# Performance work log

Measured on AMD Instinct MI355X. Metric: run time of the kernel, lower is better.

## Reference

```python
import jax, jax.numpy as jnp
import numpy as np

EPS = 1e-06
FOCUSING_FACTOR = 3


def setup_inputs() -> dict:
    key = jax.random.key(0)
    k1, k2, k3, k4, k5 = jax.random.split(key, 5)
    N, L, H, D = 8, 4096, 8, 64
    return {
        "queries": jax.random.normal(k1, (N, L, H, D), dtype=jnp.float32),
        "keys": jax.random.normal(k2, (N, L, H, D), dtype=jnp.float32),
        "values": jax.random.normal(k3, (N, L, H, D), dtype=jnp.float32),
        "scale_param": jnp.zeros((1, 1, 1, D), dtype=jnp.float32),
        "dwc_w": jax.random.normal(k4, (D, 1, 5, 5), dtype=jnp.float32) * 0.1,
        "dwc_b": jax.random.normal(k5, (D,), dtype=jnp.float32) * 0.1,
        "height": 64,
    }


def reference(queries, keys, values, scale_param, dwc_w, dwc_b, height):
    N, L, H, D = values.shape
    width = L // height

    scale = jax.nn.softplus(scale_param)  # [1,1,1,D]
    q = (jax.nn.relu(queries) + 1e-06) / scale
    k = (jax.nn.relu(keys) + 1e-06) / scale

    q_norm = jnp.linalg.norm(q, axis=-1, keepdims=True)
    k_norm = jnp.linalg.norm(k, axis=-1, keepdims=True)
    q = q ** FOCUSING_FACTOR
    k = k ** FOCUSING_FACTOR
    q = q / jnp.linalg.norm(q, axis=-1, keepdims=True) * q_norm
    k = k / jnp.linalg.norm(k, axis=-1, keepdims=True) * k_norm

    # linear attention: kv summary [N,H,D,D], normalizer z [N,L,H]
    kv = jnp.einsum("nshd,nshv->nhdv", k, values)
    z = 1.0 / (jnp.einsum("nlhd,nhd->nlh", q, k.sum(axis=1)) + EPS)
    o = jnp.einsum("nlhd,nhdv,nlh->nlhv", q, kv, z)

    # depthwise 5x5 conv on values: 'n (h w) heads d -> (n heads) d h w'
    vf = values.reshape(N, height, width, H, D)
    vf = vf.transpose(0, 3, 4, 1, 2).reshape(N * H, D, height, width)
    vf = jax.lax.conv_general_dilated(
        vf, dwc_w,
        window_strides=(1, 1), padding=((2, 2), (2, 2)),
        dimension_numbers=("NCHW", "OIHW", "NCHW"),
        feature_group_count=D,
    ) + dwc_b[None, :, None, None]
    vf = vf.reshape(N, H, D, height, width).transpose(0, 3, 4, 1, 2)
    vf = vf.reshape(N, L, H, D)

    return o + vf
```

## Files before the change

kernel.cpp:

```cpp
#include <hip/hip_runtime.h>

typedef __attribute__((ext_vector_type(8))) short short8;
typedef __attribute__((ext_vector_type(4))) float f32x4;

#define LSEQ   4096
#define NHEAD  8
#define DCH    64
#define HEIGHT 64
#define WIDTH  64

static __device__ __forceinline__ float bfu2f(unsigned short u) {
  return __uint_as_float(((unsigned int)u) << 16);
}
static __device__ __forceinline__ unsigned short f2bfu(float f) {
  unsigned int b = __float_as_uint(f);
  b += 0x7FFFu + ((b >> 16) & 1u);
  return (unsigned short)(b >> 16);
}
static __device__ __forceinline__ float ldf(const void* p, int i, int isbf) {
  return isbf ? bfu2f(((const unsigned short*)p)[i]) : ((const float*)p)[i];
}
static __device__ __forceinline__ float softplus_inv(float sp) {
  float s = (sp > 20.f) ? sp : log1pf(expf(sp));
  return 1.f / s;
}
static __device__ __forceinline__ void unpack2(unsigned int u, float& lo, float& hi) {
  lo = __uint_as_float(u << 16);
  hi = __uint_as_float(u & 0xFFFF0000u);
}
static __device__ __forceinline__ void load8(const void* p, int gi, int isbf, float o[8]) {
  if (isbf) {
    uint4 u = *(const uint4*)((const unsigned short*)p + gi);
    unpack2(u.x, o[0], o[1]); unpack2(u.y, o[2], o[3]);
    unpack2(u.z, o[4], o[5]); unpack2(u.w, o[6], o[7]);
  } else {
    const float4* f4 = (const float4*)((const float*)p + gi);
    float4 a = f4[0], b = f4[1];
    o[0]=a.x; o[1]=a.y; o[2]=a.z; o[3]=a.w;
    o[4]=b.x; o[5]=b.y; o[6]=b.z; o[7]=b.w;
  }
}
static __device__ __forceinline__ void row_reduce2(float& a, float& b) {
  #pragma unroll
  for (int m = 1; m < 8; m <<= 1) { a += __shfl_xor(a, m, 64); b += __shfl_xor(b, m, 64); }
}
static __device__ __forceinline__ float row_reduce1(float a) {
  #pragma unroll
  for (int m = 1; m < 8; m <<= 1) a += __shfl_xor(a, m, 64);
  return a;
}

__global__ void detect_kernel(const unsigned int* __restrict__ q, int* __restrict__ flag) {
  int lane = threadIdx.x & 63;
  int hits = 0;
  #pragma unroll
  for (int i = 0; i < 4; ++i) {
    unsigned int lo = q[lane * 4 + i] & 0xFFFFu;
    unsigned int e  = (lo >> 7) & 0xFFu;
    if (lo == 0u || (e >= 110u && e <= 140u)) hits++;
  }
  #pragma unroll
  for (int m = 1; m < 64; m <<= 1) hits += __shfl_xor(hits, m, 64);
  if (lane == 0) *flag = (hits > 128) ? 1 : 0;
}

__global__ __launch_bounds__(256) void kv_kernel(
    const void* __restrict__ keys, const void* __restrict__ values,
    const void* __restrict__ scale_param,
    float* __restrict__ kv_p, float* __restrict__ ksum_g,
    const int* __restrict__ flagp, int chunks, int rows)
{
  __shared__ __align__(16) unsigned short kfT[2][64 * 40];
  __shared__ __align__(16) unsigned short vvT[2][64 * 40];
  __shared__ float red[256];

  const int isbf = *flagp;
  const int b = blockIdx.x;
  const int chunk = b % chunks;
  const int nh = b / chunks;
  const int h = nh & 7, n = nh >> 3;
  const int t = threadIdx.x, lane = t & 63, wid = t >> 6;
  const int quad = lane >> 4, m16 = lane & 15;
  const int r = lane >> 3, c = lane & 7, d0 = c * 8;
  const int s_local = wid * 8 + r;
  const int sp = s_local ^ ((c & 3) << 3);

  float inv_s[8];
  #pragma unroll
  for (int i = 0; i < 8; ++i) inv_s[i] = softplus_inv(ldf(scale_param, d0 + i, isbf));

  f32x4 acc[4];
  #pragma unroll
  for (int mt = 0; mt < 4; ++mt) acc[mt] = (f32x4){0.f, 0.f, 0.f, 0.f};
  float ksum_acc[8];
  #pragma unroll
  for (int i = 0; i < 8; ++i) ksum_acc[i] = 0.f;

  const int nsub = rows >> 5;

  auto norm_k = [&](const float kraw[8], int buf) {
    float xv[8], yv[8], s2 = 0.f, s6 = 0.f;
    #pragma unroll
    for (int i = 0; i < 8; ++i) {
      xv[i] = (fmaxf(kraw[i], 0.f) + 1e-6f) * inv_s[i];
      s2 += xv[i] * xv[i];
    }
    #pragma unroll
    for (int i = 0; i < 8; ++i) {
      yv[i] = xv[i] * xv[i] * xv[i];
      s6 += yv[i] * yv[i];
    }
    row_reduce2(s2, s6);
    const float coef = sqrtf(s2 / s6);
    #pragma unroll
    for (int i = 0; i < 8; ++i) {
      float f = yv[i] * coef;
      ksum_acc[i] += f;
      kfT[buf][(d0 + i) * 40 + sp] = f2bfu(f);
    }
  };
  auto procb = [&](uint4 K, uint4 V, int buf) {
    float kraw[8];
    unpack2(K.x, kraw[0], kraw[1]); unpack2(K.y, kraw[2], kraw[3]);
    unpack2(K.z, kraw[4], kraw[5]); unpack2(K.w, kraw[6], kraw[7]);
    norm_k(kraw, buf);
    unsigned short vs8[8];
    *(uint4*)vs8 = V;
    #pragma unroll
    for (int i = 0; i < 8; ++i) vvT[buf][(d0 + i) * 40 + sp] = vs8[i];
  };
  auto mfma_step = [&](int buf) {
    const int v = wid * 16 + m16;
    short8 bfr = *(const short8*)&vvT[buf][v * 40 + (quad ^ ((v >> 3) & 3)) * 8];
    #pragma unroll
    for (int mt = 0; mt < 4; ++mt) {
      int d = mt * 16 + m16;
      short8 afr = *(const short8*)&kfT[buf][d * 40 + (quad ^ ((d >> 3) & 3)) * 8];
      acc[mt] = __builtin_amdgcn_mfma_f32_16x16x32_bf16(afr, bfr, acc[mt], 0, 0, 0);
    }
  };

  if (isbf) {
    const unsigned short* kp = (const unsigned short*)keys;
    const unsigned short* vp = (const unsigned short*)values;
    uint4 k0, k1, k2, k3, v0, v1, v2, v3;
    for (int g = 0; g < nsub; g += 4) {
      const int s = chunk * rows + g * 32 + s_local;
      const size_t gi = ((size_t)(n * LSEQ + s) * NHEAD + h) * DCH + d0;
      k0 = *(const uint4*)(kp + gi);
      v0 = *(const uint4*)(vp + gi);
      k1 = *(const uint4*)(kp + gi + 16384);
      v1 = *(const uint4*)(vp + gi + 16384);
      k2 = *(const uint4*)(kp + gi + 32768);
      v2 = *(const uint4*)(vp + gi + 32768);
      k3 = *(const uint4*)(kp + gi + 49152);
      v3 = *(const uint4*)(vp + gi + 49152);
      procb(k0, v0, 0); __syncthreads();
      mfma_step(0); procb(k1, v1, 1); __syncthreads();
      mfma_step(1); procb(k2, v2, 0); __syncthreads();
      mfma_step(0); procb(k3, v3, 1); __syncthreads();
      mfma_step(1);
    }
  } else {
    for (int sub = 0; sub < nsub; ++sub) {
      const int s = chunk * rows + sub * 32 + s_local;
      const int gi = ((n * LSEQ + s) * NHEAD + h) * DCH + d0;
      float kraw[8];
      load8(keys, gi, 0, kraw);
      norm_k(kraw, 0);
      float vraw[8];
      load8(values, gi, 0, vraw);
      #pragma unroll
      for (int i = 0; i < 8; ++i) vvT[0][(d0 + i) * 40 + sp] = f2bfu(vraw[i]);
      __syncthreads();
      mfma_step(0);
      __syncthreads();
    }
  }

  float* dst = kv_p + ((size_t)chunk * 64 + nh) * 4096;
  #pragma unroll
  for (int mt = 0; mt < 4; ++mt)
    #pragma unroll
    for (int rr = 0; rr < 4; ++rr) {
      int d = mt * 16 + quad * 4 + rr;
      dst[d * 64 + wid * 16 + m16] = acc[mt][rr];
    }

  #pragma unroll
  for (int i = 0; i < 8; ++i) {
    #pragma unroll
    for (int m = 8; m < 64; m <<= 1) ksum_acc[i] += __shfl_xor(ksum_acc[i], m, 64);
  }
  if (r == 0) {
    #pragma unroll
    for (int i = 0; i < 8; ++i) red[wid * 64 + d0 + i] = ksum_acc[i];
  }
  __syncthreads();
  if (t < 64) {
    float tot = red[t] + red[64 + t] + red[128 + t] + red[192 + t];
    atomicAdd(&ksum_g[nh * 64 + t], tot);
  }
}

__global__ __launch_bounds__(256) void reduce_kernel(
    const float* __restrict__ kv_p, unsigned short* __restrict__ kvb, int chunks)
{
  int cidx = blockIdx.x * 256 + threadIdx.x;
  int nh = cidx >> 12;
  int dv = cidx & 4095;
  int d = dv >> 6, v = dv & 63;
  float s = 0.f;
  for (int ch = 0; ch < chunks; ++ch)
    s += kv_p[((size_t)ch * 64 + nh) * 4096 + dv];
  kvb[(nh * 64 + v) * 64 + d] = f2bfu(s);
}

__global__ __launch_bounds__(256) void attn_kernel(
    const void* __restrict__ queries, const unsigned short* __restrict__ kvb,
    const float* __restrict__ ksum_g, const void* __restrict__ scale_param,
    void* __restrict__ out, const int* __restrict__ flagp)
{
  __shared__ __align__(16) unsigned short qf[64 * 72];

  const int isbf = *flagp;
  const int b = blockIdx.x;
  const int y = b & 63;
  const int nh = b >> 6;
  const int h = nh & 7, n = nh >> 3;
  const int t = threadIdx.x, lane = t & 63, wid = t >> 6;
  const int quad = lane >> 4, m16 = lane & 15;
  const int r = lane >> 3, c = lane & 7, d0 = c * 8;

  float inv_s[8];
  #pragma unroll
  for (int i = 0; i < 8; ++i) inv_s[i] = softplus_inv(ldf(scale_param, d0 + i, isbf));
  float ks[8];
  {
    float4 k0 = *(const float4*)&ksum_g[nh * 64 + d0];
    float4 k1 = *(const float4*)&ksum_g[nh * 64 + d0 + 4];
    ks[0]=k0.x; ks[1]=k0.y; ks[2]=k0.z; ks[3]=k0.w;
    ks[4]=k1.x; ks[5]=k1.y; ks[6]=k1.z; ks[7]=k1.w;
  }

  const unsigned short* kvrow = kvb + (nh * 64 + wid * 16 + m16) * 64;
  short8 bfr0 = *(const short8*)&kvrow[quad * 8];
  short8 bfr1 = *(const short8*)&kvrow[32 + quad * 8];

  #pragma unroll
  for (int batch = 0; batch < 2; ++batch) {
    int x = wid * 16 + batch * 8 + r;
    int gi = ((n * LSEQ + y * 64 + x) * NHEAD + h) * DCH + d0;
    float qraw[8];
    load8(queries, gi, isbf, qraw);
    float xv[8], yv[8], s2 = 0.f, s6 = 0.f;
    #pragma unroll
    for (int i = 0; i < 8; ++i) {
      xv[i] = (fmaxf(qraw[i], 0.f) + 1e-6f) * inv_s[i];
      s2 += xv[i] * xv[i];
    }
    #pragma unroll
    for (int i = 0; i < 8; ++i) {
      yv[i] = xv[i] * xv[i] * xv[i];
      s6 += yv[i] * yv[i];
    }
    row_reduce2(s2, s6);
    const float coef = sqrtf(s2 / s6);
    float f[8], dot = 0.f;
    #pragma unroll
    for (int i = 0; i < 8; ++i) { f[i] = yv[i] * coef; dot += f[i] * ks[i]; }
    dot = row_reduce1(dot);
    const float z = 1.f / (dot + 1e-6f);
    uint4 pk;
    pk.x = (unsigned int)f2bfu(f[0] * z) | ((unsigned int)f2bfu(f[1] * z) << 16);
    pk.y = (unsigned int)f2bfu(f[2] * z) | ((unsigned int)f2bfu(f[3] * z) << 16);
    pk.z = (unsigned int)f2bfu(f[4] * z) | ((unsigned int)f2bfu(f[5] * z) << 16);
    pk.w = (unsigned int)f2bfu(f[6] * z) | ((unsigned int)f2bfu(f[7] * z) << 16);
    *(uint4*)&qf[x * 72 + d0] = pk;
  }
  __syncthreads();

  const size_t obase = (((size_t)n * LSEQ + y * 64) * NHEAD + h) * DCH;
  #pragma unroll
  for (int mt = 0; mt < 4; ++mt) {
    f32x4 acc = (f32x4){0.f, 0.f, 0.f, 0.f};
    short8 a0 = *(const short8*)&qf[(mt * 16 + m16) * 72 + quad * 8];
    short8 a1 = *(const short8*)&qf[(mt * 16 + m16) * 72 + 32 + quad * 8];
    acc = __builtin_amdgcn_mfma_f32_16x16x32_bf16(a0, bfr0, acc, 0, 0, 0);
    acc = __builtin_amdgcn_mfma_f32_16x16x32_bf16(a1, bfr1, acc, 0, 0, 0);
    #pragma unroll
    for (int rr = 0; rr < 4; ++rr) {
      int x = mt * 16 + quad * 4 + rr;
      int v = wid * 16 + m16;
      size_t oi = obase + (size_t)x * (NHEAD * DCH) + v;
      if (isbf) ((unsigned short*)out)[oi] = f2bfu(acc[rr]);
      else      ((float*)out)[oi] = acc[rr];
    }
  }
}

__global__ __launch_bounds__(256) void conv_kernel(
    const void* __restrict__ values, const void* __restrict__ dwc_w,
    const void* __restrict__ dwc_b, void* __restrict__ out,
    const int* __restrict__ flagp)
{
  __shared__ __align__(16) unsigned short vs[8 * 64 * 32];
  __shared__ float wl[25 * 32];
  __shared__ float bl[32];

  const int isbf = *flagp;
  const int b = blockIdx.x;
  const int slab = b & 15;
  const int half = (b >> 4) & 1;
  const int nh = b >> 5;
  const int h = nh & 7, n = nh >> 3;
  const int y0 = slab * 4;
  const int t = threadIdx.x;

  for (int i = t; i < 800; i += 256) {
    int dloc = i / 25, tap = i - dloc * 25;
    wl[tap * 32 + dloc] = ldf(dwc_w, half * 800 + i, isbf);
  }
  if (t < 32) bl[t] = ldf(dwc_b, half * 32 + t, isbf);

  for (int it = t; it < 8 * 64 * 4; it += 256) {
    int j = it & 3;
    int xx = (it >> 2) & 63;
    int rr = it >> 8;
    int yy = y0 - 2 + rr;
    int swz = j ^ (xx & 3) ^ ((xx >> 2) & 3);
    unsigned short* dst = &vs[((rr * 64 + xx) * 32) + swz * 8];
    if (yy >= 0 && yy < HEIGHT) {
      int gi = ((n * LSEQ + yy * 64 + xx) * NHEAD + h) * DCH + half * 32 + j * 8;
      if (isbf) {
        *(uint4*)dst = *(const uint4*)((const unsigned short*)values + gi);
      } else {
        const float4* s4 = (const float4*)((const float*)values + gi);
        float4 f0 = s4[0], f1 = s4[1];
        dst[0] = f2bfu(f0.x); dst[1] = f2bfu(f0.y);
        dst[2] = f2bfu(f0.z); dst[3] = f2bfu(f0.w);
        dst[4] = f2bfu(f1.x); dst[5] = f2bfu(f1.y);
        dst[6] = f2bfu(f1.z); dst[7] = f2bfu(f1.w);
      }
    } else {
      uint4 z; z.x = z.y = z.z = z.w = 0u;
      *(uint4*)dst = z;
    }
  }
  __syncthreads();

  const int xx = t >> 2, jb = t & 3;
  float a[4][8];
  float bias8[8];
  {
    float4 b0 = *(const float4*)&bl[jb * 8];
    float4 b1 = *(const float4*)&bl[jb * 8 + 4];
    bias8[0]=b0.x; bias8[1]=b0.y; bias8[2]=b0.z; bias8[3]=b0.w;
    bias8[4]=b1.x; bias8[5]=b1.y; bias8[6]=b1.z; bias8[7]=b1.w;
  }
  #pragma unroll
  for (int rr = 0; rr < 4; ++rr)
    #pragma unroll
    for (int cc = 0; cc < 8; ++cc) a[rr][cc] = bias8[cc];

  for (int ky = 0; ky < 5; ++ky) {
    #pragma unroll
    for (int kx = 0; kx < 5; ++kx) {
      int xs = xx + kx - 2;
      if ((unsigned)xs < (unsigned)WIDTH) {
        float4 w0 = *(const float4*)&wl[(ky * 5 + kx) * 32 + jb * 8];
        float4 w1 = *(const float4*)&wl[(ky * 5 + kx) * 32 + jb * 8 + 4];
        int swz = jb ^ (xs & 3) ^ ((xs >> 2) & 3);
        #pragma unroll
        for (int rr = 0; rr < 4; ++rr) {
          uint4 pv = *(const uint4*)&vs[(((rr + ky) * 64 + xs) * 32) + swz * 8];
          float v0,v1,v2,v3,v4,v5,v6,v7;
          unpack2(pv.x, v0, v1); unpack2(pv.y, v2, v3);
          unpack2(pv.z, v4, v5); unpack2(pv.w, v6, v7);
          a[rr][0] += w0.x * v0; a[rr][1] += w0.y * v1;
          a[rr][2] += w0.z * v2; a[rr][3] += w0.w * v3;
          a[rr][4] += w1.x * v4; a[rr][5] += w1.y * v5;
          a[rr][6] += w1.z * v6; a[rr][7] += w1.w * v7;
        }
      }
    }
  }
  #pragma unroll
  for (int rr = 0; rr < 4; ++rr) {
    size_t oi = (((size_t)n * LSEQ + (y0 + rr) * 64 + xx) * NHEAD + h) * DCH
              + half * 32 + jb * 8;
    if (isbf) {
      unsigned short* op = (unsigned short*)out + oi;
      uint4 cur = *(uint4*)op;
      float c0,c1,c2,c3,c4,c5,c6,c7;
      unpack2(cur.x, c0, c1); unpack2(cur.y, c2, c3);
      unpack2(cur.z, c4, c5); unpack2(cur.w, c6, c7);
      uint4 res;
      res.x = (unsigned int)f2bfu(c0 + a[rr][0]) | ((unsigned int)f2bfu(c1 + a[rr][1]) << 16);
      res.y = (unsigned int)f2bfu(c2 + a[rr][2]) | ((unsigned int)f2bfu(c3 + a[rr][3]) << 16);
      res.z = (unsigned int)f2bfu(c4 + a[rr][4]) | ((unsigned int)f2bfu(c5 + a[rr][5]) << 16);
      res.w = (unsigned int)f2bfu(c6 + a[rr][6]) | ((unsigned int)f2bfu(c7 + a[rr][7]) << 16);
      *(uint4*)op = res;
    } else {
      float* op = (float*)out + oi;
      float4 o0 = *(float4*)op;
      float4 o1 = *(float4*)(op + 4);
      o0.x += a[rr][0]; o0.y += a[rr][1]; o0.z += a[rr][2]; o0.w += a[rr][3];
      o1.x += a[rr][4]; o1.y += a[rr][5]; o1.z += a[rr][6]; o1.w += a[rr][7];
      *(float4*)op = o0;
      *(float4*)(op + 4) = o1;
    }
  }
}

extern "C" void kernel_launch(void* const* d_in, const int* in_sizes, int n_in,
                              void* d_out, int out_size, void* d_ws, size_t ws_size,
                              hipStream_t stream) {
  int chunks = 32;
  while (chunks > 1) {
    size_t need = (size_t)chunks * 64 * 4096 * 4 + 64 * 4096 * 2 + 4096 * 4 + 64;
    if (need <= ws_size) break;
    chunks >>= 1;
  }
  const int rows = LSEQ / chunks;

  float* kv_p = (float*)d_ws;
  unsigned short* kvb = (unsigned short*)(kv_p + (size_t)chunks * 64 * 4096);
  float* ksum = (float*)(kvb + 64 * 4096);
  int* flag = (int*)(ksum + 4096);

  hipMemsetAsync(ksum, 0, 4096 * sizeof(float), stream);
  detect_kernel<<<1, 64, 0, stream>>>((const unsigned int*)d_in[0], flag);
  kv_kernel<<<64 * chunks, 256, 0, stream>>>(
      d_in[1], d_in[2], d_in[3], kv_p, ksum, flag, chunks, rows);
  reduce_kernel<<<1024, 256, 0, stream>>>(kv_p, kvb, chunks);
  attn_kernel<<<4096, 256, 0, stream>>>(
      d_in[0], kvb, ksum, d_in[3], d_out, flag);
  conv_kernel<<<64 * 32, 256, 0, stream>>>(
      d_in[2], d_in[4], d_in[5], d_out, flag);
}
```

Before: 315.6 us.

## Batch four sub-tiles per barrier in kv_kernel and halve chunk count

The kv_kernel now stages four 32-row sub-tiles into four LDS buffers and then runs one MFMA round over all of them. This replaces the per-sub-tile double-buffered ping-pong and cuts the barriers from four to two per group. The fp32 path is restructured the same way. Chunks drop from 32 to 16, which halves the partial kv buffers and reduce work but doubles the rows per block and halves the grid. LDS use doubles, and there is less overlap between normalization and MFMA.

```diff
diff --git a/kernel.cpp b/kernel.cpp
--- a/kernel.cpp
+++ b/kernel.cpp
@@ -70,8 +70,8 @@
     float* __restrict__ kv_p, float* __restrict__ ksum_g,
     const int* __restrict__ flagp, int chunks, int rows)
 {
-  __shared__ __align__(16) unsigned short kfT[2][64 * 40];
-  __shared__ __align__(16) unsigned short vvT[2][64 * 40];
+  __shared__ __align__(16) unsigned short kfT[4][64 * 40];
+  __shared__ __align__(16) unsigned short vvT[4][64 * 40];
   __shared__ float red[256];
 
   const int isbf = *flagp;
@@ -98,7 +98,7 @@
 
   const int nsub = rows >> 5;
 
-  auto norm_k = [&](const float kraw[8], int buf) {
+  auto norm_k = [&](const float kraw[8], int sub) {
     float xv[8], yv[8], s2 = 0.f, s6 = 0.f;
     #pragma unroll
     for (int i = 0; i < 8; ++i) {
@@ -116,27 +116,30 @@
     for (int i = 0; i < 8; ++i) {
       float f = yv[i] * coef;
       ksum_acc[i] += f;
-      kfT[buf][(d0 + i) * 40 + sp] = f2bfu(f);
+      kfT[sub][(d0 + i) * 40 + sp] = f2bfu(f);
     }
   };
-  auto procb = [&](uint4 K, uint4 V, int buf) {
+  auto procb = [&](uint4 K, uint4 V, int sub) {
     float kraw[8];
     unpack2(K.x, kraw[0], kraw[1]); unpack2(K.y, kraw[2], kraw[3]);
     unpack2(K.z, kraw[4], kraw[5]); unpack2(K.w, kraw[6], kraw[7]);
-    norm_k(kraw, buf);
+    norm_k(kraw, sub);
     unsigned short vs8[8];
     *(uint4*)vs8 = V;
     #pragma unroll
-    for (int i = 0; i < 8; ++i) vvT[buf][(d0 + i) * 40 + sp] = vs8[i];
+    for (int i = 0; i < 8; ++i) vvT[sub][(d0 + i) * 40 + sp] = vs8[i];
   };
-  auto mfma_step = [&](int buf) {
+  auto mfma_round = [&]() {
     const int v = wid * 16 + m16;
-    short8 bfr = *(const short8*)&vvT[buf][v * 40 + (quad ^ ((v >> 3) & 3)) * 8];
-    #pragma unroll
-    for (int mt = 0; mt < 4; ++mt) {
-      int d = mt * 16 + m16;
-      short8 afr = *(const short8*)&kfT[buf][d * 40 + (quad ^ ((d >> 3) & 3)) * 8];
-      acc[mt] = __builtin_amdgcn_mfma_f32_16x16x32_bf16(afr, bfr, acc[mt], 0, 0, 0);
+    #pragma unroll
+    for (int ks = 0; ks < 4; ++ks) {
+      short8 bfr = *(const short8*)&vvT[ks][v * 40 + (quad ^ ((v >> 3) & 3)) * 8];
+      #pragma unroll
+      for (int mt = 0; mt < 4; ++mt) {
+        int d = mt * 16 + m16;
+        short8 afr = *(const short8*)&kfT[ks][d * 40 + (quad ^ ((d >> 3) & 3)) * 8];
+        acc[mt] = __builtin_amdgcn_mfma_f32_16x16x32_bf16(afr, bfr, acc[mt], 0, 0, 0);
+      }
     }
   };
 
@@ -155,25 +158,30 @@
       v2 = *(const uint4*)(vp + gi + 32768);
       k3 = *(const uint4*)(kp + gi + 49152);
       v3 = *(const uint4*)(vp + gi + 49152);
-      procb(k0, v0, 0); __syncthreads();
-      mfma_step(0); procb(k1, v1, 1); __syncthreads();
-      mfma_step(1); procb(k2, v2, 0); __syncthreads();
-      mfma_step(0); procb(k3, v3, 1); __syncthreads();
-      mfma_step(1);
+      procb(k0, v0, 0);
+      procb(k1, v1, 1);
+      procb(k2, v2, 2);
+      procb(k3, v3, 3);
+      __syncthreads();
+      mfma_round();
+      __syncthreads();
     }
   } else {
-    for (int sub = 0; sub < nsub; ++sub) {
-      const int s = chunk * rows + sub * 32 + s_local;
-      const int gi = ((n * LSEQ + s) * NHEAD + h) * DCH + d0;
-      float kraw[8];
-      load8(keys, gi, 0, kraw);
-      norm_k(kraw, 0);
-      float vraw[8];
-      load8(values, gi, 0, vraw);
+    for (int g = 0; g < nsub; g += 4) {
       #pragma unroll
-      for (int i = 0; i < 8; ++i) vvT[0][(d0 + i) * 40 + sp] = f2bfu(vraw[i]);
+      for (int sub = 0; sub < 4; ++sub) {
+        const int s = chunk * rows + (g + sub) * 32 + s_local;
+        const int gi = ((n * LSEQ + s) * NHEAD + h) * DCH + d0;
+        float kraw[8];
+        load8(keys, gi, 0, kraw);
+        norm_k(kraw, sub);
+        float vraw[8];
+        load8(values, gi, 0, vraw);
+        #pragma unroll
+        for (int i = 0; i < 8; ++i) vvT[sub][(d0 + i) * 40 + sp] = f2bfu(vraw[i]);
+      }
       __syncthreads();
-      mfma_step(0);
+      mfma_round();
       __syncthreads();
     }
   }
@@ -416,7 +424,7 @@
 extern "C" void kernel_launch(void* const* d_in, const int* in_sizes, int n_in,
                               void* d_out, int out_size, void* d_ws, size_t ws_size,
                               hipStream_t stream) {
-  int chunks = 32;
+  int chunks = 16;
   while (chunks > 1) {
     size_t need = (size_t)chunks * 64 * 4096 * 4 + 64 * 4096 * 2 + 4096 * 4 + 64;
     if (need <= ws_size) break;
```

Measured after the change: 316.3 us. No clear change (+0.2%).
